# Kernel tuning notes

Measured on AMD Instinct MI355X. Metric: run time of the kernel, lower is better.

The kernel has to match this reference:

```python
import jax, jax.numpy as jnp
import numpy as np
from jax import lax

B, L = 8, 1024
C_IN, D_MODEL = 3, 512
N_MAMBA, N_TRANS, NHEAD = 2, 2, 8
D_STATE, D_CONV, EXPAND = 16, 4, 2
DI = EXPAND * D_MODEL            # 1024, mamba inner dim
DT_RANK = D_MODEL // 16          # 32
DH = D_MODEL // NHEAD            # 64, head dim
DFF = 4 * D_MODEL


def setup_inputs() -> dict:
    key = jax.random.key(0)
    ks = iter(jax.random.split(key, 64))
    def rn(shape, s=0.05):
        return jax.random.normal(next(ks), shape, jnp.float32) * s
    inp = {
        'x': jax.random.normal(next(ks), (B, C_IN, L), jnp.float32),
        'proj_w': rn((D_MODEL, C_IN)), 'proj_b': rn((D_MODEL,)),
        # stacked per-mamba-layer params (leading dim = N_MAMBA)
        'm_in_w': rn((N_MAMBA, 2 * DI, D_MODEL)),
        'm_conv_w': rn((N_MAMBA, DI, D_CONV)), 'm_conv_b': rn((N_MAMBA, DI)),
        'm_xproj_w': rn((N_MAMBA, DT_RANK + 2 * D_STATE, DI)),
        'm_dt_w': rn((N_MAMBA, DI, DT_RANK)), 'm_dt_b': rn((N_MAMBA, DI)),
        'm_Alog': jnp.tile(jnp.log(jnp.arange(1, D_STATE + 1, dtype=jnp.float32)), (N_MAMBA, DI, 1)),
        'm_D': jnp.ones((N_MAMBA, DI), jnp.float32),
        'm_out_w': rn((N_MAMBA, D_MODEL, DI)),
        'm_ln_w': jnp.ones((N_MAMBA, D_MODEL), jnp.float32), 'm_ln_b': jnp.zeros((N_MAMBA, D_MODEL), jnp.float32),
        # stacked per-transformer-layer params
        't_qkv_w': rn((N_TRANS, 3 * D_MODEL, D_MODEL)), 't_qkv_b': rn((N_TRANS, 3 * D_MODEL)),
        't_ow': rn((N_TRANS, D_MODEL, D_MODEL)), 't_ob': rn((N_TRANS, D_MODEL)),
        't_l1w': rn((N_TRANS, DFF, D_MODEL)), 't_l1b': rn((N_TRANS, DFF)),
        't_l2w': rn((N_TRANS, D_MODEL, DFF)), 't_l2b': rn((N_TRANS, D_MODEL)),
        't_ln1w': jnp.ones((N_TRANS, D_MODEL), jnp.float32), 't_ln1b': jnp.zeros((N_TRANS, D_MODEL), jnp.float32),
        't_ln2w': jnp.ones((N_TRANS, D_MODEL), jnp.float32), 't_ln2b': jnp.zeros((N_TRANS, D_MODEL), jnp.float32),
        'no_w': jnp.ones((D_MODEL,), jnp.float32), 'no_b': jnp.zeros((D_MODEL,), jnp.float32),
    }
    return inp


def _ln(x, w, b, eps=1e-5):
    m = x.mean(-1, keepdims=True)
    v = ((x - m) ** 2).mean(-1, keepdims=True)
    return (x - m) / jnp.sqrt(v + eps) * w + b


def _pos_encoding(length, d):
    pos = jnp.arange(length, dtype=jnp.float32)[:, None]
    div = jnp.exp(jnp.arange(0, d, 2, dtype=jnp.float32) * (-np.log(10000.0) / d))
    pe = jnp.zeros((length, d), jnp.float32)
    pe = pe.at[:, 0::2].set(jnp.sin(pos * div)).at[:, 1::2].set(jnp.cos(pos * div))
    return pe


def _mamba(h, in_w, conv_w, conv_b, xp_w, dt_w, dt_b, Alog, Dp, out_w):
    # h: [B,L,d_model]
    xz = h @ in_w.T                                   # [B,L,2*DI]
    xm, z = jnp.split(xz, 2, axis=-1)
    # causal depthwise conv1d over time
    k = conv_w.T[:, None, :]                          # [D_CONV,1,DI]
    xc = lax.conv_general_dilated(xm, k, (1,), [(D_CONV - 1, 0)],
                                  dimension_numbers=('NWC', 'WIO', 'NWC'),
                                  feature_group_count=DI) + conv_b
    xc = jax.nn.silu(xc)
    xdb = xc @ xp_w.T                                 # [B,L,DT_RANK+2*D_STATE]
    dt = jax.nn.softplus(xdb[..., :DT_RANK] @ dt_w.T + dt_b)   # [B,L,DI]
    Bm = xdb[..., DT_RANK:DT_RANK + D_STATE]          # [B,L,D_STATE]
    Cm = xdb[..., DT_RANK + D_STATE:]                 # [B,L,D_STATE]
    A = -jnp.exp(Alog)                                # [DI,D_STATE]

    def step(state, t):
        dt_t, B_t, C_t, x_t = t                       # [B,DI],[B,S],[B,S],[B,DI]
        dA = jnp.exp(dt_t[..., None] * A)             # [B,DI,S]
        state = state * dA + (dt_t * x_t)[..., None] * B_t[:, None, :]
        y = jnp.einsum('bds,bs->bd', state, C_t)
        return state, y

    init = jnp.zeros((h.shape[0], DI, D_STATE), h.dtype)
    seq = (dt.transpose(1, 0, 2), Bm.transpose(1, 0, 2), Cm.transpose(1, 0, 2), xc.transpose(1, 0, 2))
    _, ys = lax.scan(step, init, seq)                 # ys: [L,B,DI]
    y = ys.transpose(1, 0, 2) + Dp * xc
    y = y * jax.nn.silu(z)
    return y @ out_w.T                                # [B,L,d_model]


def _transformer_layer(h, qkv_w, qkv_b, ow, ob, l1w, l1b, l2w, l2b, ln1w, ln1b, ln2w, ln2b):
    Bt, Lt, d = h.shape
    qkv = h @ qkv_w.T + qkv_b
    q, k, v = jnp.split(qkv, 3, axis=-1)
    q = q.reshape(Bt, Lt, NHEAD, DH); k = k.reshape(Bt, Lt, NHEAD, DH); v = v.reshape(Bt, Lt, NHEAD, DH)
    sc = jnp.einsum('blhd,bmhd->bhlm', q, k) / np.sqrt(DH).astype(np.float32)
    a = jax.nn.softmax(sc, axis=-1)
    o = jnp.einsum('bhlm,bmhd->blhd', a, v).reshape(Bt, Lt, d)
    h = _ln(h + o @ ow.T + ob, ln1w, ln1b)
    ff = jax.nn.relu(h @ l1w.T + l1b) @ l2w.T + l2b
    return _ln(h + ff, ln2w, ln2b)


def reference(x, proj_w, proj_b, m_in_w, m_conv_w, m_conv_b, m_xproj_w, m_dt_w, m_dt_b,
              m_Alog, m_D, m_out_w, m_ln_w, m_ln_b, t_qkv_w, t_qkv_b, t_ow, t_ob,
              t_l1w, t_l1b, t_l2w, t_l2b, t_ln1w, t_ln1b, t_ln2w, t_ln2b, no_w, no_b):
    # proj_in: 1x1 conv == pointwise linear over channels; output [B,L,d]
    h = jnp.einsum('bcl,dc->bld', x, proj_w) + proj_b
    for i in range(N_MAMBA):
        h = _ln(h + _mamba(h, m_in_w[i], m_conv_w[i], m_conv_b[i], m_xproj_w[i],
                           m_dt_w[i], m_dt_b[i], m_Alog[i], m_D[i], m_out_w[i]),
                m_ln_w[i], m_ln_b[i])
    h = h + _pos_encoding(h.shape[1], D_MODEL)
    for i in range(N_TRANS):
        h = _transformer_layer(h, t_qkv_w[i], t_qkv_b[i], t_ow[i], t_ob[i],
                               t_l1w[i], t_l1b[i], t_l2w[i], t_l2b[i],
                               t_ln1w[i], t_ln1b[i], t_ln2w[i], t_ln2b[i])
    h = _ln(h, no_w, no_b)
    return h, h.mean(axis=1)
```

## Files before the change

kernel.cpp:

```cpp
#include <hip/hip_runtime.h>
#include <cstddef>

#define BATCH 8
#define LSEQ 1024
#define DMODEL 512
#define DINNER 1024
#define DSTATE 16
#define DTRANK 32
#define NHEAD 8
#define DHEAD 64
#define DFF 2048
#define MTOK 8192
#define NCHUNK 16
#define CLEN 64

typedef __attribute__((ext_vector_type(8))) short bfrag;
typedef __attribute__((ext_vector_type(4))) float f32x4;
typedef __attribute__((ext_vector_type(4))) unsigned short us4;
typedef unsigned short ushort_t;

__device__ __forceinline__ float silu_f(float x) { return x / (1.f + __expf(-x)); }

__device__ __forceinline__ unsigned short f2bf(float f) {
  unsigned u = __float_as_uint(f);
  return (unsigned short)((u + 0x7FFFu + ((u >> 16) & 1u)) >> 16);
}
__device__ __forceinline__ float bf2f(ushort_t u) {
  return __uint_as_float((unsigned)u << 16);
}

__device__ __forceinline__ void gll16(const ushort_t* g, ushort_t* l) {
  __builtin_amdgcn_global_load_lds(
      (const __attribute__((address_space(1))) unsigned int*)g,
      (__attribute__((address_space(3))) unsigned int*)l, 16, 0, 0);
}

__global__ __launch_bounds__(256) void cvt_bf16(const float* __restrict__ s,
                                                ushort_t* __restrict__ d, int n4) {
  int i = blockIdx.x * 256 + threadIdx.x;
  if (i >= n4) return;
  float4 v = ((const float4*)s)[i];
  us4 o = {f2bf(v.x), f2bf(v.y), f2bf(v.z), f2bf(v.w)};
  ((us4*)d)[i] = o;
}

__global__ __launch_bounds__(256) void proj_kernel(const float* __restrict__ x,
                                                   const float* __restrict__ pw,
                                                   const float* __restrict__ pb,
                                                   float* __restrict__ h,
                                                   ushort_t* __restrict__ hbf) {
  int idx = blockIdx.x * 256 + threadIdx.x;
  int d = idx & 511;
  int l = (idx >> 9) & 1023;
  int b = idx >> 19;
  const float* xb = x + (size_t)b * 3 * 1024 + l;
  float v = pb[d] + xb[0] * pw[d * 3] + xb[1024] * pw[d * 3 + 1] + xb[2048] * pw[d * 3 + 2];
  h[idx] = v;
  hbf[idx] = f2bf(v);
}

template <int ACT, int CBF, int SPLITK, int BN>
__global__ __launch_bounds__(256) void gemm_gll(const ushort_t* __restrict__ A,
                                                const ushort_t* __restrict__ W,
                                                const float* __restrict__ bias,
                                                void* __restrict__ Cp,
                                                int K, int lda, int ldc) {
  __shared__ ushort_t sA[2][4096];
  __shared__ ushort_t sB[2][BN * 32];
  constexpr int MREP = (BN == 128) ? 4 : 2;
  const int bm = blockIdx.y * 128, bn = blockIdx.x * BN;
  const int tid = threadIdx.x;
  const int wid = tid >> 6, lane = tid & 63;
  const int wrb = (BN == 128) ? (wid >> 1) * 64 : wid * 32;
  const int wcb = (BN == 128) ? (wid & 1) * 64 : 0;
  const int lr = lane & 15, ls = lane >> 4;
  const int sw = ls ^ ((lr >> 1) & 3);

  const int kseg = K / SPLITK;
  const int kbeg = (SPLITK > 1) ? blockIdx.z * kseg : 0;

  const int c0 = wid * 128 + lane;
  const int c1 = c0 + 64;
  const int r0 = c0 >> 2, s0 = (c0 & 3) ^ ((r0 >> 1) & 3);
  const int r1 = c1 >> 2, s1 = (c1 & 3) ^ ((r1 >> 1) & 3);
  const ushort_t* gA0 = A + (size_t)(bm + r0) * lda + kbeg + s0 * 8;
  const ushort_t* gA1 = A + (size_t)(bm + r1) * lda + kbeg + s1 * 8;
  const ushort_t* gB0;
  const ushort_t* gB1 = nullptr;
  if constexpr (BN == 128) {
    gB0 = W + (size_t)(bn + r0) * K + kbeg + s0 * 8;
    gB1 = W + (size_t)(bn + r1) * K + kbeg + s1 * 8;
  } else {
    const int cb = wid * 64 + lane;
    const int rb = cb >> 2, sb2 = (cb & 3) ^ ((rb >> 1) & 3);
    gB0 = W + (size_t)(bn + rb) * K + kbeg + sb2 * 8;
  }

  f32x4 acc[MREP][4];
#pragma unroll
  for (int i = 0; i < MREP; ++i)
#pragma unroll
    for (int j = 0; j < 4; ++j) acc[i][j] = (f32x4)(0.f);

#define STAGE(buf, step)                                             \
  do {                                                               \
    gll16(gA0 + (step) * 32, &sA[buf][wid * 1024]);                  \
    gll16(gA1 + (step) * 32, &sA[buf][wid * 1024 + 512]);            \
    if constexpr (BN == 128) {                                       \
      gll16(gB0 + (step) * 32, &sB[buf][wid * 1024]);                \
      gll16(gB1 + (step) * 32, &sB[buf][wid * 1024 + 512]);          \
    } else {                                                         \
      gll16(gB0 + (step) * 32, &sB[buf][wid * 512]);                 \
    }                                                                \
  } while (0)

  const int NT = kseg / 32;
  STAGE(0, 0);
  for (int t = 0; t < NT; ++t) {
    const int cur = t & 1;
    if (t + 1 < NT) {
      STAGE(cur ^ 1, t + 1);
      if constexpr (BN == 128)
        asm volatile("s_waitcnt vmcnt(4)" ::: "memory");
      else
        asm volatile("s_waitcnt vmcnt(3)" ::: "memory");
    } else {
      asm volatile("s_waitcnt vmcnt(0)" ::: "memory");
    }
    __builtin_amdgcn_sched_barrier(0);
    __builtin_amdgcn_s_barrier();
    __builtin_amdgcn_sched_barrier(0);

    bfrag af[MREP], bf[4];
#pragma unroll
    for (int mi = 0; mi < MREP; ++mi) {
      int row = wrb + mi * 16 + lr;
      af[mi] = *(const bfrag*)&sA[cur][(size_t)((row << 2) + sw) * 8];
    }
#pragma unroll
    for (int nj = 0; nj < 4; ++nj) {
      int col = wcb + nj * 16 + lr;
      bf[nj] = *(const bfrag*)&sB[cur][(size_t)((col << 2) + sw) * 8];
    }
#pragma unroll
    for (int mi = 0; mi < MREP; ++mi)
#pragma unroll
      for (int nj = 0; nj < 4; ++nj)
        acc[mi][nj] = __builtin_amdgcn_mfma_f32_16x16x32_bf16(af[mi], bf[nj], acc[mi][nj], 0, 0, 0);

    __builtin_amdgcn_s_barrier();
    __builtin_amdgcn_sched_barrier(0);
  }
#undef STAGE

  if (SPLITK > 1) {
    float* Cz = (float*)Cp + (size_t)blockIdx.z * 8192 * ldc;
#pragma unroll
    for (int nj = 0; nj < 4; ++nj) {
      int col = bn + wcb + nj * 16 + lr;
#pragma unroll
      for (int mi = 0; mi < MREP; ++mi) {
        int row0 = bm + wrb + mi * 16 + ls * 4;
#pragma unroll
        for (int r = 0; r < 4; ++r)
          Cz[(size_t)(row0 + r) * ldc + col] = acc[mi][nj][r];
      }
    }
  } else {
#pragma unroll
    for (int nj = 0; nj < 4; ++nj) {
      int col = bn + wcb + nj * 16 + lr;
      float bv = bias ? bias[col] : 0.f;
#pragma unroll
      for (int mi = 0; mi < MREP; ++mi) {
        int row0 = bm + wrb + mi * 16 + ls * 4;
#pragma unroll
        for (int r = 0; r < 4; ++r) {
          float v = acc[mi][nj][r] + bv;
          if (ACT == 1) v = fmaxf(v, 0.f);
          if (ACT == 2) v = (v > 20.f) ? v : log1pf(__expf(v));
          if (CBF)
            ((ushort_t*)Cp)[(size_t)(row0 + r) * ldc + col] = f2bf(v);
          else
            ((float*)Cp)[(size_t)(row0 + r) * ldc + col] = v;
        }
      }
    }
  }
}

__global__ __launch_bounds__(256) void splitk_reduce(const float* __restrict__ p,
                                                     const float* __restrict__ bias,
                                                     float* __restrict__ out) {
  int i = blockIdx.x * 256 + threadIdx.x;
  float4 a = ((const float4*)p)[i];
  float4 b = ((const float4*)p)[i + 1048576];
  float4 o = {a.x + b.x, a.y + b.y, a.z + b.z, a.w + b.w};
  if (bias) {
    float4 bb = ((const float4*)bias)[i & 127];
    o.x += bb.x; o.y += bb.y; o.z += bb.z; o.w += bb.w;
  }
  ((float4*)out)[i] = o;
}

__global__ __launch_bounds__(256) void reduce8_xdb(const float* __restrict__ p,
                                                   float* __restrict__ xdb,
                                                   ushort_t* __restrict__ xdb_bf) {
  int i = blockIdx.x * 256 + threadIdx.x;
  float4 a = ((const float4*)p)[i];
#pragma unroll
  for (int z = 1; z < 8; ++z) {
    float4 b = ((const float4*)p)[i + z * 131072];
    a.x += b.x; a.y += b.y; a.z += b.z; a.w += b.w;
  }
  ((float4*)xdb)[i] = a;
  us4 o = {f2bf(a.x), f2bf(a.y), f2bf(a.z), f2bf(a.w)};
  ((us4*)xdb_bf)[i] = o;
}

__global__ __launch_bounds__(256) void conv_silu_kernel(const float* __restrict__ xz,
                                                        const float* __restrict__ cw,
                                                        const float* __restrict__ cb,
                                                        ushort_t* __restrict__ xc) {
  int idx = blockIdx.x * 256 + threadIdx.x;
  int d = idx & 1023;
  int t = (idx >> 10) & 1023;
  int b = idx >> 20;
  float acc = cb[d];
#pragma unroll
  for (int w = 0; w < 4; ++w) {
    int tt = t - 3 + w;
    if (tt >= 0) acc += xz[(((size_t)(b * 1024 + tt)) << 11) + d] * cw[d * 4 + w];
  }
  xc[idx] = f2bf(silu_f(acc));
}

__global__ __launch_bounds__(256) void scan_pass1(const float* __restrict__ dt,
                                                  const float* __restrict__ xdb,
                                                  const ushort_t* __restrict__ xc,
                                                  const float* __restrict__ Alog,
                                                  float* __restrict__ scrP,
                                                  float* __restrict__ scrL) {
  int idx = blockIdx.x * 256 + threadIdx.x;
  int sh = idx & 3;
  int d = (idx >> 2) & 1023;
  int c = (idx >> 12) & 15;
  int b = idx >> 16;
  float A[4], st[4], P[4];
#pragma unroll
  for (int s = 0; s < 4; ++s) {
    A[s] = -__expf(Alog[d * 16 + sh * 4 + s]);
    st[s] = 0.f;
    P[s] = 1.f;
  }
  int t0 = c * CLEN;
  size_t base = (((size_t)(b * 1024 + t0)) << 10) + d;
  const float* xb = xdb + (size_t)(b * 1024 + t0) * 64 + 32 + sh * 4;
  float dtv = dt[base], xv = bf2f(xc[base]);
  for (int t = 0; t < CLEN; ++t) {
    float dtn = 0.f, xvn = 0.f;
    if (t + 1 < CLEN) { dtn = dt[base + 1024]; xvn = bf2f(xc[base + 1024]); }
    float4 Bv = *(const float4*)xb;
    float dx = dtv * xv;
    float e0 = __expf(dtv * A[0]), e1 = __expf(dtv * A[1]);
    float e2 = __expf(dtv * A[2]), e3 = __expf(dtv * A[3]);
    st[0] = st[0] * e0 + dx * Bv.x; P[0] *= e0;
    st[1] = st[1] * e1 + dx * Bv.y; P[1] *= e1;
    st[2] = st[2] * e2 + dx * Bv.z; P[2] *= e2;
    st[3] = st[3] * e3 + dx * Bv.w; P[3] *= e3;
    base += 1024; xb += 64;
    dtv = dtn; xv = xvn;
  }
  size_t pbase = (((size_t)((b * 16 + c) * 16 + sh * 4)) << 10) + d;
#pragma unroll
  for (int s = 0; s < 4; ++s) {
    scrP[pbase + ((size_t)s << 10)] = P[s];
    scrL[pbase + ((size_t)s << 10)] = st[s];
  }
}

__global__ __launch_bounds__(256) void scan_pass2(const float* __restrict__ scrP,
                                                  float* __restrict__ scrL) {
  int idx = blockIdx.x * 256 + threadIdx.x;
  int d = idx & 1023;
  int s = (idx >> 10) & 15;
  int b = idx >> 14;
  float cur = 0.f;
  for (int c = 0; c < 16; ++c) {
    size_t o = (((size_t)(((b * 16 + c) * 16) + s)) << 10) + d;
    float P = scrP[o];
    float loc = scrL[o];
    scrL[o] = cur;
    cur = cur * P + loc;
  }
}

__global__ __launch_bounds__(256) void scan_pass3(const float* __restrict__ dt,
                                                  const float* __restrict__ xdb,
                                                  const ushort_t* __restrict__ xc,
                                                  const float* __restrict__ xz,
                                                  ushort_t* __restrict__ ybf,
                                                  const float* __restrict__ Alog,
                                                  const float* __restrict__ Dp,
                                                  const float* __restrict__ scrL) {
  int idx = blockIdx.x * 256 + threadIdx.x;
  int sh = idx & 3;
  int d = (idx >> 2) & 1023;
  int c = (idx >> 12) & 15;
  int b = idx >> 16;
  float A[4], st[4];
  size_t pbase = (((size_t)((b * 16 + c) * 16 + sh * 4)) << 10) + d;
#pragma unroll
  for (int s = 0; s < 4; ++s) {
    A[s] = -__expf(Alog[d * 16 + sh * 4 + s]);
    st[s] = scrL[pbase + ((size_t)s << 10)];
  }
  float Dv = Dp[d];
  int t0 = c * CLEN;
  size_t base = (((size_t)(b * 1024 + t0)) << 10) + d;
  size_t zoff = ((((size_t)(b * 1024 + t0)) << 11)) + 1024 + d;
  const float* xb = xdb + (size_t)(b * 1024 + t0) * 64 + 32 + sh * 4;
  float dtv = dt[base], xv = bf2f(xc[base]), zv = xz[zoff];
  for (int t = 0; t < CLEN; ++t) {
    float dtn = 0.f, xvn = 0.f, zvn = 0.f;
    if (t + 1 < CLEN) {
      dtn = dt[base + 1024]; xvn = bf2f(xc[base + 1024]); zvn = xz[zoff + 2048];
    }
    float4 Bv = *(const float4*)xb;
    float4 Cv = *(const float4*)(xb + 16);
    float dx = dtv * xv;
    float e0 = __expf(dtv * A[0]), e1 = __expf(dtv * A[1]);
    float e2 = __expf(dtv * A[2]), e3 = __expf(dtv * A[3]);
    st[0] = st[0] * e0 + dx * Bv.x;
    st[1] = st[1] * e1 + dx * Bv.y;
    st[2] = st[2] * e2 + dx * Bv.z;
    st[3] = st[3] * e3 + dx * Bv.w;
    float acc = st[0] * Cv.x + st[1] * Cv.y + st[2] * Cv.z + st[3] * Cv.w;
    acc += __shfl_xor(acc, 1);
    acc += __shfl_xor(acc, 2);
    if (sh == 0)
      ybf[base] = f2bf((acc + Dv * xv) * silu_f(zv));
    base += 1024; zoff += 2048; xb += 64;
    dtv = dtn; xv = xvn; zv = zvn;
  }
}

__global__ __launch_bounds__(128) void resid_ln_kernel(const float* __restrict__ x,
                                                       const float* __restrict__ add,
                                                       const float* __restrict__ w,
                                                       const float* __restrict__ bias,
                                                       float* __restrict__ out,
                                                       ushort_t* __restrict__ out_bf) {
  int row = blockIdx.x, tid = threadIdx.x;
  float4 v = ((const float4*)(x + (size_t)row * 512))[tid];
  if (add) {
    float4 a = ((const float4*)(add + (size_t)row * 512))[tid];
    v.x += a.x; v.y += a.y; v.z += a.z; v.w += a.w;
  }
  float s = v.x + v.y + v.z + v.w;
  float ss = v.x * v.x + v.y * v.y + v.z * v.z + v.w * v.w;
#pragma unroll
  for (int o = 32; o; o >>= 1) {
    s += __shfl_xor(s, o);
    ss += __shfl_xor(ss, o);
  }
  __shared__ float red[4];
  int wid = tid >> 6;
  if ((tid & 63) == 0) { red[wid] = s; red[2 + wid] = ss; }
  __syncthreads();
  s = red[0] + red[1];
  ss = red[2] + red[3];
  float mean = s * (1.f / 512.f);
  float var = ss * (1.f / 512.f) - mean * mean;
  float inv = rsqrtf(var + 1e-5f);
  float4 wv = ((const float4*)w)[tid];
  float4 bv = ((const float4*)bias)[tid];
  float4 ov;
  ov.x = (v.x - mean) * inv * wv.x + bv.x;
  ov.y = (v.y - mean) * inv * wv.y + bv.y;
  ov.z = (v.z - mean) * inv * wv.z + bv.z;
  ov.w = (v.w - mean) * inv * wv.w + bv.w;
  ((float4*)(out + (size_t)row * 512))[tid] = ov;
  if (out_bf) {
    us4 ob = {f2bf(ov.x), f2bf(ov.y), f2bf(ov.z), f2bf(ov.w)};
    ((us4*)(out_bf + (size_t)row * 512))[tid] = ob;
  }
}

__global__ __launch_bounds__(256) void posenc_kernel(float* __restrict__ h,
                                                     ushort_t* __restrict__ hbf) {
  int idx = blockIdx.x * 256 + threadIdx.x;
  int d = idx & 511;
  int l = (idx >> 9) & 1023;
  float freq = __expf(-(float)(d & ~1) * (9.210340371976184f / 512.f));
  float ang = (float)l * freq;
  float v = h[idx] + ((d & 1) ? cosf(ang) : sinf(ang));
  h[idx] = v;
  hbf[idx] = f2bf(v);
}

__global__ __launch_bounds__(256) void attn_mfma(const ushort_t* __restrict__ qkv,
                                                 ushort_t* __restrict__ ao) {
  __shared__ unsigned short Qs[4096];
  __shared__ unsigned short Ks[4096];
  __shared__ unsigned short Vt[4096];
  __shared__ unsigned short Ps[4096];
  const int tid = threadIdx.x;
  const int blk = blockIdx.x;
  const int qt = blk & 15, hh = (blk >> 4) & 7, b = blk >> 7;
  const int l0 = qt * 64;
  const size_t bb = (size_t)b * 1024 * 1536;

  const int srow = tid >> 2;
  const int sdb = (tid & 3) << 4;
  const int sc0 = sdb >> 3;

  {
    const ushort_t* qp = qkv + bb + (size_t)(l0 + srow) * 1536 + hh * 64 + sdb;
    *(bfrag*)&Qs[srow * 64 + ((sc0 ^ (srow & 7)) << 3)] = *(const bfrag*)qp;
    *(bfrag*)&Qs[srow * 64 + (((sc0 + 1) ^ (srow & 7)) << 3)] = *(const bfrag*)(qp + 8);
  }

  const int wid = tid >> 6, lane = tid & 63;
  const int l15 = lane & 15, rg = lane >> 4;
  const int l7 = l15 & 7;
  float m[4], lsum[4];
  f32x4 oacc[4];
#pragma unroll
  for (int r = 0; r < 4; ++r) { m[r] = -1e30f; lsum[r] = 0.f; }
#pragma unroll
  for (int nt = 0; nt < 4; ++nt) oacc[nt] = (f32x4)(0.f);

  for (int jt = 0; jt < 16; ++jt) {
    {
      const ushort_t* kp = qkv + bb + (size_t)(jt * 64 + srow) * 1536 + hh * 64 + 512 + sdb;
      *(bfrag*)&Ks[srow * 64 + ((sc0 ^ (srow & 7)) << 3)] = *(const bfrag*)kp;
      *(bfrag*)&Ks[srow * 64 + (((sc0 + 1) ^ (srow & 7)) << 3)] = *(const bfrag*)(kp + 8);
      const ushort_t* vp = kp + 512;
      unsigned short vv[16];
      *(bfrag*)&vv[0] = *(const bfrag*)vp;
      *(bfrag*)&vv[8] = *(const bfrag*)(vp + 8);
#pragma unroll
      for (int j = 0; j < 16; ++j) {
        int dd = sdb + j;
        Vt[dd * 64 + (((srow >> 3) ^ (dd & 7)) << 3) + (srow & 7)] = vv[j];
      }
    }
    __syncthreads();

    bfrag aq[2];
#pragma unroll
    for (int ks = 0; ks < 2; ++ks)
      aq[ks] = *(const bfrag*)&Qs[(wid * 16 + l15) * 64 + (((ks * 4 + rg) ^ l7) << 3)];
    f32x4 sc[4];
#pragma unroll
    for (int nt = 0; nt < 4; ++nt) {
      f32x4 s = (f32x4)(0.f);
#pragma unroll
      for (int ks = 0; ks < 2; ++ks) {
        bfrag bk = *(const bfrag*)&Ks[(nt * 16 + l15) * 64 + (((ks * 4 + rg) ^ l7) << 3)];
        s = __builtin_amdgcn_mfma_f32_16x16x32_bf16(aq[ks], bk, s, 0, 0, 0);
      }
      sc[nt] = s * 0.125f;
    }

#pragma unroll
    for (int r = 0; r < 4; ++r) {
      float mc = fmaxf(fmaxf(sc[0][r], sc[1][r]), fmaxf(sc[2][r], sc[3][r]));
#pragma unroll
      for (int o = 8; o; o >>= 1) mc = fmaxf(mc, __shfl_xor(mc, o));
      float mn = fmaxf(m[r], mc);
      float al = __expf(m[r] - mn);
      m[r] = mn;
      int prow = rg * 4 + r;
      float ps = 0.f;
#pragma unroll
      for (int nt = 0; nt < 4; ++nt) {
        float p = __expf(sc[nt][r] - mn);
        ps += p;
        int col = nt * 16 + l15;
        Ps[wid * 1024 + prow * 64 + ((((col >> 3) ^ (prow & 7))) << 3) + (col & 7)] = f2bf(p);
      }
#pragma unroll
      for (int o = 8; o; o >>= 1) ps += __shfl_xor(ps, o);
      lsum[r] = lsum[r] * al + ps;
#pragma unroll
      for (int nt = 0; nt < 4; ++nt) oacc[nt][r] *= al;
    }

    bfrag ap[2];
#pragma unroll
    for (int ks = 0; ks < 2; ++ks)
      ap[ks] = *(const bfrag*)&Ps[wid * 1024 + l15 * 64 + (((ks * 4 + rg) ^ l7) << 3)];
#pragma unroll
    for (int nt = 0; nt < 4; ++nt) {
#pragma unroll
      for (int ks = 0; ks < 2; ++ks) {
        bfrag bv = *(const bfrag*)&Vt[(nt * 16 + l15) * 64 + (((ks * 4 + rg) ^ l7) << 3)];
        oacc[nt] = __builtin_amdgcn_mfma_f32_16x16x32_bf16(ap[ks], bv, oacc[nt], 0, 0, 0);
      }
    }
    __syncthreads();
  }

#pragma unroll
  for (int r = 0; r < 4; ++r) {
    float inv = 1.f / lsum[r];
    int row = l0 + wid * 16 + rg * 4 + r;
    ushort_t* op = ao + ((size_t)(b * 1024 + row)) * 512 + hh * 64;
#pragma unroll
    for (int nt = 0; nt < 4; ++nt) op[nt * 16 + l15] = f2bf(oacc[nt][r] * inv);
  }
}

__global__ __launch_bounds__(512) void mean_part(const float* __restrict__ h,
                                                 float* __restrict__ part) {
  int blk = blockIdx.x;
  int b = blk >> 4, lc = blk & 15, d = threadIdx.x;
  float s = 0.f;
  int l0 = lc * 64;
  for (int l = l0; l < l0 + 64; ++l) s += h[(((size_t)(b * 1024 + l)) << 9) + d];
  part[((size_t)blk << 9) + d] = s;
}
__global__ __launch_bounds__(256) void mean_final(const float* __restrict__ part,
                                                  float* __restrict__ out2) {
  int i = blockIdx.x * 256 + threadIdx.x;
  int b = i >> 9, d = i & 511;
  float s = 0.f;
#pragma unroll
  for (int c = 0; c < 16; ++c) s += part[(((size_t)(b * 16 + c)) << 9) + d];
  out2[i] = s * (1.f / 1024.f);
}

extern "C" void kernel_launch(void* const* d_in, const int* in_sizes, int n_in,
                              void* d_out, int out_size, void* d_ws, size_t ws_size,
                              hipStream_t stream) {
  const float* x        = (const float*)d_in[0];
  const float* proj_w   = (const float*)d_in[1];
  const float* proj_b   = (const float*)d_in[2];
  const float* m_in_w   = (const float*)d_in[3];
  const float* m_conv_w = (const float*)d_in[4];
  const float* m_conv_b = (const float*)d_in[5];
  const float* m_xproj_w= (const float*)d_in[6];
  const float* m_dt_w   = (const float*)d_in[7];
  const float* m_dt_b   = (const float*)d_in[8];
  const float* m_Alog   = (const float*)d_in[9];
  const float* m_D      = (const float*)d_in[10];
  const float* m_out_w  = (const float*)d_in[11];
  const float* m_ln_w   = (const float*)d_in[12];
  const float* m_ln_b   = (const float*)d_in[13];
  const float* t_qkv_w  = (const float*)d_in[14];
  const float* t_qkv_b  = (const float*)d_in[15];
  const float* t_ow     = (const float*)d_in[16];
  const float* t_ob     = (const float*)d_in[17];
  const float* t_l1w    = (const float*)d_in[18];
  const float* t_l1b    = (const float*)d_in[19];
  const float* t_l2w    = (const float*)d_in[20];
  const float* t_l2b    = (const float*)d_in[21];
  const float* t_ln1w   = (const float*)d_in[22];
  const float* t_ln1b   = (const float*)d_in[23];
  const float* t_ln2w   = (const float*)d_in[24];
  const float* t_ln2b   = (const float*)d_in[25];
  const float* no_w     = (const float*)d_in[26];
  const float* no_b     = (const float*)d_in[27];

  float* ws   = (float*)d_ws;
  float* h    = ws;
  ushort_t* h_bf = (ushort_t*)(ws + 4194304);
  float* bufA = ws + 6291456;
  float* bufB = bufA + 16777216;
  float* bufC = bufB + 8388608;
  float* bufE = bufC + 8388608;
  float* bufF = bufE + 4194304;
  ushort_t* y_bf = (ushort_t*)(bufF + 524288);
  ushort_t* wbf  = (ushort_t*)(bufF + 524288 + 4194304);
  float* scrP = bufE;
  float* scrL = bufE + 2097152;

  ushort_t* wIN  = wbf;
  ushort_t* wOUT = wbf + 2097152;
  ushort_t* wQKV = wbf + 3145728;
  ushort_t* wOW  = wbf + 4718592;
  ushort_t* wL1  = wbf + 5242880;
  ushort_t* wL2  = wbf + 7340032;
  ushort_t* wXP  = wbf + 9437184;
  ushort_t* wDT  = wbf + 9568256;
  ushort_t* xdb_bf = wbf + 9633792;

  cvt_bf16<<<2048, 256, 0, stream>>>(m_in_w,  wIN,  524288);
  cvt_bf16<<<1024, 256, 0, stream>>>(m_out_w, wOUT, 262144);
  cvt_bf16<<<1536, 256, 0, stream>>>(t_qkv_w, wQKV, 393216);
  cvt_bf16<<< 512, 256, 0, stream>>>(t_ow,    wOW,  131072);
  cvt_bf16<<<2048, 256, 0, stream>>>(t_l1w,   wL1,  524288);
  cvt_bf16<<<2048, 256, 0, stream>>>(t_l2w,   wL2,  524288);
  cvt_bf16<<< 128, 256, 0, stream>>>(m_xproj_w, wXP, 32768);
  cvt_bf16<<<  64, 256, 0, stream>>>(m_dt_w,  wDT,  16384);

  proj_kernel<<<16384, 256, 0, stream>>>(x, proj_w, proj_b, h, h_bf);

  for (int i = 0; i < 2; ++i) {
    gemm_gll<0, 0, 1, 128><<<dim3(16, 64), 256, 0, stream>>>(
        h_bf, wIN + (size_t)i * 1048576, nullptr, bufA, DMODEL, DMODEL, 2 * DINNER);
    conv_silu_kernel<<<32768, 256, 0, stream>>>(bufA, m_conv_w + i * DINNER * 4,
                                                m_conv_b + i * DINNER, (ushort_t*)bufB);
    gemm_gll<0, 0, 8, 64><<<dim3(1, 64, 8), 256, 0, stream>>>(
        (const ushort_t*)bufB, wXP + (size_t)i * 65536, nullptr, bufC,
        DINNER, DINNER, 64);
    reduce8_xdb<<<512, 256, 0, stream>>>(bufC, bufF, xdb_bf);
    gemm_gll<2, 0, 1, 128><<<dim3(8, 64), 256, 0, stream>>>(
        xdb_bf, wDT + (size_t)i * 32768, m_dt_b + i * DINNER, bufC,
        DTRANK, 64, DINNER);
    scan_pass1<<<2048, 256, 0, stream>>>(bufC, bufF, (const ushort_t*)bufB,
                                         m_Alog + (size_t)i * DINNER * DSTATE, scrP, scrL);
    scan_pass2<<<512, 256, 0, stream>>>(scrP, scrL);
    scan_pass3<<<2048, 256, 0, stream>>>(bufC, bufF, (const ushort_t*)bufB, bufA, y_bf,
                                         m_Alog + (size_t)i * DINNER * DSTATE,
                                         m_D + i * DINNER, scrL);
    gemm_gll<0, 0, 2, 128><<<dim3(4, 64, 2), 256, 0, stream>>>(
        y_bf, wOUT + (size_t)i * 524288, nullptr, bufC, DINNER, DINNER, DMODEL);
    splitk_reduce<<<4096, 256, 0, stream>>>(bufC, nullptr, bufE);
    resid_ln_kernel<<<8192, 128, 0, stream>>>(h, bufE, m_ln_w + i * DMODEL,
                                              m_ln_b + i * DMODEL, h, h_bf);
  }

  posenc_kernel<<<16384, 256, 0, stream>>>(h, h_bf);

  for (int i = 0; i < 2; ++i) {
    gemm_gll<0, 1, 1, 128><<<dim3(12, 64), 256, 0, stream>>>(
        h_bf, wQKV + (size_t)i * 786432, t_qkv_b + i * 3 * DMODEL, bufA,
        DMODEL, DMODEL, 3 * DMODEL);
    attn_mfma<<<1024, 256, 0, stream>>>((const ushort_t*)bufA, (ushort_t*)bufB);
    gemm_gll<0, 0, 2, 128><<<dim3(4, 64, 2), 256, 0, stream>>>(
        (const ushort_t*)bufB, wOW + (size_t)i * 262144, nullptr, bufC,
        DMODEL, DMODEL, DMODEL);
    splitk_reduce<<<4096, 256, 0, stream>>>(bufC, t_ob + i * DMODEL, bufE);
    resid_ln_kernel<<<8192, 128, 0, stream>>>(h, bufE, t_ln1w + i * DMODEL,
                                              t_ln1b + i * DMODEL, h, h_bf);
    gemm_gll<1, 1, 1, 128><<<dim3(16, 64), 256, 0, stream>>>(
        h_bf, wL1 + (size_t)i * 1048576, t_l1b + i * DFF, bufA,
        DMODEL, DMODEL, DFF);
    gemm_gll<0, 0, 2, 128><<<dim3(4, 64, 2), 256, 0, stream>>>(
        (const ushort_t*)bufA, wL2 + (size_t)i * 1048576, nullptr, bufC,
        DFF, DFF, DMODEL);
    splitk_reduce<<<4096, 256, 0, stream>>>(bufC, t_l2b + i * DMODEL, bufE);
    resid_ln_kernel<<<8192, 128, 0, stream>>>(h, bufE, t_ln2w + i * DMODEL,
                                              t_ln2b + i * DMODEL, h, h_bf);
  }

  float* out_h = (float*)d_out;
  resid_ln_kernel<<<8192, 128, 0, stream>>>(h, nullptr, no_w, no_b, out_h, nullptr);
  mean_part<<<128, 512, 0, stream>>>(out_h, bufF);
  mean_final<<<16, 256, 0, stream>>>(bufF, out_h + 4194304);
}
```

Measured before the change: 987.4 us.

## Fuse split-K reduce into residual LayerNorm, store in_proj as bf16, widen attention tiles

The separate split-K reduction kernel is removed. Its two partial sums and the bias are now added inside a new residual-LayerNorm kernel, which saves one full-size write and read of the activation per linear layer. The Mamba in_proj GEMM now writes bf16 instead of fp32, so the conv and scan kernels read half the bytes, at the cost of rounding the gate and input values. The attention kernel now handles 128 query rows per block with each wave covering two 16-row sub-tiles, so every K/V tile loaded into shared memory is reused twice. This uses more registers and launches half as many blocks.

Measured after the change: 963.8 us. 1.02x faster.

```diff
diff --git a/kernel.cpp b/kernel.cpp
--- a/kernel.cpp
+++ b/kernel.cpp
@@ -189,20 +189,6 @@
   }
 }
 
-__global__ __launch_bounds__(256) void splitk_reduce(const float* __restrict__ p,
-                                                     const float* __restrict__ bias,
-                                                     float* __restrict__ out) {
-  int i = blockIdx.x * 256 + threadIdx.x;
-  float4 a = ((const float4*)p)[i];
-  float4 b = ((const float4*)p)[i + 1048576];
-  float4 o = {a.x + b.x, a.y + b.y, a.z + b.z, a.w + b.w};
-  if (bias) {
-    float4 bb = ((const float4*)bias)[i & 127];
-    o.x += bb.x; o.y += bb.y; o.z += bb.z; o.w += bb.w;
-  }
-  ((float4*)out)[i] = o;
-}
-
 __global__ __launch_bounds__(256) void reduce8_xdb(const float* __restrict__ p,
                                                    float* __restrict__ xdb,
                                                    ushort_t* __restrict__ xdb_bf) {
@@ -218,7 +204,7 @@
   ((us4*)xdb_bf)[i] = o;
 }
 
-__global__ __launch_bounds__(256) void conv_silu_kernel(const float* __restrict__ xz,
+__global__ __launch_bounds__(256) void conv_silu_kernel(const ushort_t* __restrict__ xz,
                                                         const float* __restrict__ cw,
                                                         const float* __restrict__ cb,
                                                         ushort_t* __restrict__ xc) {
@@ -230,7 +216,7 @@
 #pragma unroll
   for (int w = 0; w < 4; ++w) {
     int tt = t - 3 + w;
-    if (tt >= 0) acc += xz[(((size_t)(b * 1024 + tt)) << 11) + d] * cw[d * 4 + w];
+    if (tt >= 0) acc += bf2f(xz[(((size_t)(b * 1024 + tt)) << 11) + d]) * cw[d * 4 + w];
   }
   xc[idx] = f2bf(silu_f(acc));
 }
@@ -298,7 +284,7 @@
 __global__ __launch_bounds__(256) void scan_pass3(const float* __restrict__ dt,
                                                   const float* __restrict__ xdb,
                                                   const ushort_t* __restrict__ xc,
-                                                  const float* __restrict__ xz,
+                                                  const ushort_t* __restrict__ xz,
                                                   ushort_t* __restrict__ ybf,
                                                   const float* __restrict__ Alog,
                                                   const float* __restrict__ Dp,
@@ -320,11 +306,11 @@
   size_t base = (((size_t)(b * 1024 + t0)) << 10) + d;
   size_t zoff = ((((size_t)(b * 1024 + t0)) << 11)) + 1024 + d;
   const float* xb = xdb + (size_t)(b * 1024 + t0) * 64 + 32 + sh * 4;
-  float dtv = dt[base], xv = bf2f(xc[base]), zv = xz[zoff];
+  float dtv = dt[base], xv = bf2f(xc[base]), zv = bf2f(xz[zoff]);
   for (int t = 0; t < CLEN; ++t) {
     float dtn = 0.f, xvn = 0.f, zvn = 0.f;
     if (t + 1 < CLEN) {
-      dtn = dt[base + 1024]; xvn = bf2f(xc[base + 1024]); zvn = xz[zoff + 2048];
+      dtn = dt[base + 1024]; xvn = bf2f(xc[base + 1024]); zvn = bf2f(xz[zoff + 2048]);
     }
     float4 Bv = *(const float4*)xb;
     float4 Cv = *(const float4*)(xb + 16);
@@ -387,6 +373,50 @@
   }
 }
 
+__global__ __launch_bounds__(128) void resid_ln_sk(const float* __restrict__ x,
+                                                   const float* __restrict__ p,
+                                                   const float* __restrict__ pbias,
+                                                   const float* __restrict__ w,
+                                                   const float* __restrict__ bias,
+                                                   float* __restrict__ out,
+                                                   ushort_t* __restrict__ out_bf) {
+  int row = blockIdx.x, tid = threadIdx.x;
+  float4 v = ((const float4*)(x + (size_t)row * 512))[tid];
+  float4 a = ((const float4*)(p + (size_t)row * 512))[tid];
+  float4 c = ((const float4*)(p + 4194304 + (size_t)row * 512))[tid];
+  v.x += a.x + c.x; v.y += a.y + c.y; v.z += a.z + c.z; v.w += a.w + c.w;
+  if (pbias) {
+    float4 pb = ((const float4*)pbias)[tid];
+    v.x += pb.x; v.y += pb.y; v.z += pb.z; v.w += pb.w;
+  }
+  float s = v.x + v.y + v.z + v.w;
+  float ss = v.x * v.x + v.y * v.y + v.z * v.z + v.w * v.w;
+#pragma unroll
+  for (int o = 32; o; o >>= 1) {
+    s += __shfl_xor(s, o);
+    ss += __shfl_xor(ss, o);
+  }
+  __shared__ float red[4];
+  int wid = tid >> 6;
+  if ((tid & 63) == 0) { red[wid] = s; red[2 + wid] = ss; }
+  __syncthreads();
+  s = red[0] + red[1];
+  ss = red[2] + red[3];
+  float mean = s * (1.f / 512.f);
+  float var = ss * (1.f / 512.f) - mean * mean;
+  float inv = rsqrtf(var + 1e-5f);
+  float4 wv = ((const float4*)w)[tid];
+  float4 bv = ((const float4*)bias)[tid];
+  float4 ov;
+  ov.x = (v.x - mean) * inv * wv.x + bv.x;
+  ov.y = (v.y - mean) * inv * wv.y + bv.y;
+  ov.z = (v.z - mean) * inv * wv.z + bv.z;
+  ov.w = (v.w - mean) * inv * wv.w + bv.w;
+  ((float4*)(out + (size_t)row * 512))[tid] = ov;
+  us4 ob = {f2bf(ov.x), f2bf(ov.y), f2bf(ov.z), f2bf(ov.w)};
+  ((us4*)(out_bf + (size_t)row * 512))[tid] = ob;
+}
+
 __global__ __launch_bounds__(256) void posenc_kernel(float* __restrict__ h,
                                                      ushort_t* __restrict__ hbf) {
   int idx = blockIdx.x * 256 + threadIdx.x;
@@ -401,14 +431,14 @@
 
 __global__ __launch_bounds__(256) void attn_mfma(const ushort_t* __restrict__ qkv,
                                                  ushort_t* __restrict__ ao) {
-  __shared__ unsigned short Qs[4096];
+  __shared__ unsigned short Qs[8192];
   __shared__ unsigned short Ks[4096];
   __shared__ unsigned short Vt[4096];
   __shared__ unsigned short Ps[4096];
   const int tid = threadIdx.x;
   const int blk = blockIdx.x;
-  const int qt = blk & 15, hh = (blk >> 4) & 7, b = blk >> 7;
-  const int l0 = qt * 64;
+  const int qt = blk & 7, hh = (blk >> 3) & 7, b = blk >> 6;
+  const int l0 = qt * 128;
   const size_t bb = (size_t)b * 1024 * 1536;
 
   const int srow = tid >> 2;
@@ -419,17 +449,35 @@
     const ushort_t* qp = qkv + bb + (size_t)(l0 + srow) * 1536 + hh * 64 + sdb;
     *(bfrag*)&Qs[srow * 64 + ((sc0 ^ (srow & 7)) << 3)] = *(const bfrag*)qp;
     *(bfrag*)&Qs[srow * 64 + (((sc0 + 1) ^ (srow & 7)) << 3)] = *(const bfrag*)(qp + 8);
-  }
+    const ushort_t* qp2 = qp + (size_t)64 * 1536;
+    *(bfrag*)&Qs[(srow + 64) * 64 + ((sc0 ^ (srow & 7)) << 3)] = *(const bfrag*)qp2;
+    *(bfrag*)&Qs[(srow + 64) * 64 + (((sc0 + 1) ^ (srow & 7)) << 3)] = *(const bfrag*)(qp2 + 8);
+  }
+  __syncthreads();
 
   const int wid = tid >> 6, lane = tid & 63;
   const int l15 = lane & 15, rg = lane >> 4;
   const int l7 = l15 & 7;
-  float m[4], lsum[4];
-  f32x4 oacc[4];
-#pragma unroll
-  for (int r = 0; r < 4; ++r) { m[r] = -1e30f; lsum[r] = 0.f; }
-#pragma unroll
-  for (int nt = 0; nt < 4; ++nt) oacc[nt] = (f32x4)(0.f);
+
+  bfrag aq[2][2];
+#pragma unroll
+  for (int s = 0; s < 2; ++s)
+#pragma unroll
+    for (int ks = 0; ks < 2; ++ks) {
+      int qr = wid * 32 + s * 16 + l15;
+      aq[s][ks] = *(const bfrag*)&Qs[qr * 64 + (((ks * 4 + rg) ^ l7) << 3)];
+    }
+
+  float m[2][4], lsum[2][4];
+  f32x4 oacc[2][4];
+#pragma unroll
+  for (int s = 0; s < 2; ++s)
+#pragma unroll
+    for (int r = 0; r < 4; ++r) { m[s][r] = -1e30f; lsum[s][r] = 0.f; }
+#pragma unroll
+  for (int s = 0; s < 2; ++s)
+#pragma unroll
+    for (int nt = 0; nt < 4; ++nt) oacc[s][nt] = (f32x4)(0.f);
 
   for (int jt = 0; jt < 16; ++jt) {
     {
@@ -448,69 +496,70 @@
     }
     __syncthreads();
 
-    bfrag aq[2];
-#pragma unroll
-    for (int ks = 0; ks < 2; ++ks)
-      aq[ks] = *(const bfrag*)&Qs[(wid * 16 + l15) * 64 + (((ks * 4 + rg) ^ l7) << 3)];
-    f32x4 sc[4];
-#pragma unroll
-    for (int nt = 0; nt < 4; ++nt) {
-      f32x4 s = (f32x4)(0.f);
-#pragma unroll
-      for (int ks = 0; ks < 2; ++ks) {
-        bfrag bk = *(const bfrag*)&Ks[(nt * 16 + l15) * 64 + (((ks * 4 + rg) ^ l7) << 3)];
-        s = __builtin_amdgcn_mfma_f32_16x16x32_bf16(aq[ks], bk, s, 0, 0, 0);
+#pragma unroll
+    for (int s = 0; s < 2; ++s) {
+      f32x4 sc[4];
+#pragma unroll
+      for (int nt = 0; nt < 4; ++nt) {
+        f32x4 sv = (f32x4)(0.f);
+#pragma unroll
+        for (int ks = 0; ks < 2; ++ks) {
+          bfrag bk = *(const bfrag*)&Ks[(nt * 16 + l15) * 64 + (((ks * 4 + rg) ^ l7) << 3)];
+          sv = __builtin_amdgcn_mfma_f32_16x16x32_bf16(aq[s][ks], bk, sv, 0, 0, 0);
+        }
+        sc[nt] = sv * 0.125f;
       }
-      sc[nt] = s * 0.125f;
-    }
-
+
+#pragma unroll
+      for (int r = 0; r < 4; ++r) {
+        float mc = fmaxf(fmaxf(sc[0][r], sc[1][r]), fmaxf(sc[2][r], sc[3][r]));
+#pragma unroll
+        for (int o = 8; o; o >>= 1) mc = fmaxf(mc, __shfl_xor(mc, o));
+        float mn = fmaxf(m[s][r], mc);
+        float al = __expf(m[s][r] - mn);
+        m[s][r] = mn;
+        int prow = rg * 4 + r;
+        float ps = 0.f;
+#pragma unroll
+        for (int nt = 0; nt < 4; ++nt) {
+          float p = __expf(sc[nt][r] - mn);
+          ps += p;
+          int col = nt * 16 + l15;
+          Ps[wid * 1024 + prow * 64 + ((((col >> 3) ^ (prow & 7))) << 3) + (col & 7)] = f2bf(p);
+        }
+#pragma unroll
+        for (int o = 8; o; o >>= 1) ps += __shfl_xor(ps, o);
+        lsum[s][r] = lsum[s][r] * al + ps;
+#pragma unroll
+        for (int nt = 0; nt < 4; ++nt) oacc[s][nt][r] *= al;
+      }
+
+      bfrag ap[2];
+#pragma unroll
+      for (int ks = 0; ks < 2; ++ks)
+        ap[ks] = *(const bfrag*)&Ps[wid * 1024 + l15 * 64 + (((ks * 4 + rg) ^ l7) << 3)];
+#pragma unroll
+      for (int nt = 0; nt < 4; ++nt) {
+#pragma unroll
+        for (int ks = 0; ks < 2; ++ks) {
+          bfrag bv = *(const bfrag*)&Vt[(nt * 16 + l15) * 64 + (((ks * 4 + rg) ^ l7) << 3)];
+          oacc[s][nt] = __builtin_amdgcn_mfma_f32_16x16x32_bf16(ap[ks], bv, oacc[s][nt], 0, 0, 0);
+        }
+      }
+    }
+    __syncthreads();
+  }
+
+#pragma unroll
+  for (int s = 0; s < 2; ++s)
 #pragma unroll
     for (int r = 0; r < 4; ++r) {
-      float mc = fmaxf(fmaxf(sc[0][r], sc[1][r]), fmaxf(sc[2][r], sc[3][r]));
-#pragma unroll
-      for (int o = 8; o; o >>= 1) mc = fmaxf(mc, __shfl_xor(mc, o));
-      float mn = fmaxf(m[r], mc);
-      float al = __expf(m[r] - mn);
-      m[r] = mn;
-      int prow = rg * 4 + r;
-      float ps = 0.f;
-#pragma unroll
-      for (int nt = 0; nt < 4; ++nt) {
-        float p = __expf(sc[nt][r] - mn);
-        ps += p;
-        int col = nt * 16 + l15;
-        Ps[wid * 1024 + prow * 64 + ((((col >> 3) ^ (prow & 7))) << 3) + (col & 7)] = f2bf(p);
-      }
-#pragma unroll
-      for (int o = 8; o; o >>= 1) ps += __shfl_xor(ps, o);
-      lsum[r] = lsum[r] * al + ps;
-#pragma unroll
-      for (int nt = 0; nt < 4; ++nt) oacc[nt][r] *= al;
-    }
-
-    bfrag ap[2];
-#pragma unroll
-    for (int ks = 0; ks < 2; ++ks)
-      ap[ks] = *(const bfrag*)&Ps[wid * 1024 + l15 * 64 + (((ks * 4 + rg) ^ l7) << 3)];
-#pragma unroll
-    for (int nt = 0; nt < 4; ++nt) {
-#pragma unroll
-      for (int ks = 0; ks < 2; ++ks) {
-        bfrag bv = *(const bfrag*)&Vt[(nt * 16 + l15) * 64 + (((ks * 4 + rg) ^ l7) << 3)];
-        oacc[nt] = __builtin_amdgcn_mfma_f32_16x16x32_bf16(ap[ks], bv, oacc[nt], 0, 0, 0);
-      }
-    }
-    __syncthreads();
-  }
-
-#pragma unroll
-  for (int r = 0; r < 4; ++r) {
-    float inv = 1.f / lsum[r];
-    int row = l0 + wid * 16 + rg * 4 + r;
-    ushort_t* op = ao + ((size_t)(b * 1024 + row)) * 512 + hh * 64;
-#pragma unroll
-    for (int nt = 0; nt < 4; ++nt) op[nt * 16 + l15] = f2bf(oacc[nt][r] * inv);
-  }
+      float inv = 1.f / lsum[s][r];
+      int row = l0 + wid * 32 + s * 16 + rg * 4 + r;
+      ushort_t* op = ao + ((size_t)(b * 1024 + row)) * 512 + hh * 64;
+#pragma unroll
+      for (int nt = 0; nt < 4; ++nt) op[nt * 16 + l15] = f2bf(oacc[s][nt][r] * inv);
+    }
 }
 
 __global__ __launch_bounds__(512) void mean_part(const float* __restrict__ h,
@@ -599,9 +648,10 @@
   proj_kernel<<<16384, 256, 0, stream>>>(x, proj_w, proj_b, h, h_bf);
 
   for (int i = 0; i < 2; ++i) {
-    gemm_gll<0, 0, 1, 128><<<dim3(16, 64), 256, 0, stream>>>(
+    gemm_gll<0, 1, 1, 128><<<dim3(16, 64), 256, 0, stream>>>(
         h_bf, wIN + (size_t)i * 1048576, nullptr, bufA, DMODEL, DMODEL, 2 * DINNER);
-    conv_silu_kernel<<<32768, 256, 0, stream>>>(bufA, m_conv_w + i * DINNER * 4,
+    conv_silu_kernel<<<32768, 256, 0, stream>>>((const ushort_t*)bufA,
+                                                m_conv_w + i * DINNER * 4,
                                                 m_conv_b + i * DINNER, (ushort_t*)bufB);
     gemm_gll<0, 0, 8, 64><<<dim3(1, 64, 8), 256, 0, stream>>>(
         (const ushort_t*)bufB, wXP + (size_t)i * 65536, nullptr, bufC,
@@ -613,14 +663,14 @@
     scan_pass1<<<2048, 256, 0, stream>>>(bufC, bufF, (const ushort_t*)bufB,
                                          m_Alog + (size_t)i * DINNER * DSTATE, scrP, scrL);
     scan_pass2<<<512, 256, 0, stream>>>(scrP, scrL);
-    scan_pass3<<<2048, 256, 0, stream>>>(bufC, bufF, (const ushort_t*)bufB, bufA, y_bf,
+    scan_pass3<<<2048, 256, 0, stream>>>(bufC, bufF, (const ushort_t*)bufB,
+                                         (const ushort_t*)bufA, y_bf,
                                          m_Alog + (size_t)i * DINNER * DSTATE,
                                          m_D + i * DINNER, scrL);
     gemm_gll<0, 0, 2, 128><<<dim3(4, 64, 2), 256, 0, stream>>>(
         y_bf, wOUT + (size_t)i * 524288, nullptr, bufC, DINNER, DINNER, DMODEL);
-    splitk_reduce<<<4096, 256, 0, stream>>>(bufC, nullptr, bufE);
-    resid_ln_kernel<<<8192, 128, 0, stream>>>(h, bufE, m_ln_w + i * DMODEL,
-                                              m_ln_b + i * DMODEL, h, h_bf);
+    resid_ln_sk<<<8192, 128, 0, stream>>>(h, bufC, nullptr, m_ln_w + i * DMODEL,
+                                          m_ln_b + i * DMODEL, h, h_bf);
   }
 
   posenc_kernel<<<16384, 256, 0, stream>>>(h, h_bf);
@@ -629,22 +679,20 @@
     gemm_gll<0, 1, 1, 128><<<dim3(12, 64), 256, 0, stream>>>(
         h_bf, wQKV + (size_t)i * 786432, t_qkv_b + i * 3 * DMODEL, bufA,
         DMODEL, DMODEL, 3 * DMODEL);
-    attn_mfma<<<1024, 256, 0, stream>>>((const ushort_t*)bufA, (ushort_t*)bufB);
+    attn_mfma<<<512, 256, 0, stream>>>((const ushort_t*)bufA, (ushort_t*)bufB);
     gemm_gll<0, 0, 2, 128><<<dim3(4, 64, 2), 256, 0, stream>>>(
         (const ushort_t*)bufB, wOW + (size_t)i * 262144, nullptr, bufC,
         DMODEL, DMODEL, DMODEL);
-    splitk_reduce<<<4096, 256, 0, stream>>>(bufC, t_ob + i * DMODEL, bufE);
-    resid_ln_kernel<<<8192, 128, 0, stream>>>(h, bufE, t_ln1w + i * DMODEL,
-                                              t_ln1b + i * DMODEL, h, h_bf);
+    resid_ln_sk<<<8192, 128, 0, stream>>>(h, bufC, t_ob + i * DMODEL,
+                                          t_ln1w + i * DMODEL, t_ln1b + i * DMODEL, h, h_bf);
     gemm_gll<1, 1, 1, 128><<<dim3(16, 64), 256, 0, stream>>>(
         h_bf, wL1 + (size_t)i * 1048576, t_l1b + i * DFF, bufA,
         DMODEL, DMODEL, DFF);
     gemm_gll<0, 0, 2, 128><<<dim3(4, 64, 2), 256, 0, stream>>>(
         (const ushort_t*)bufA, wL2 + (size_t)i * 1048576, nullptr, bufC,
         DFF, DFF, DMODEL);
-    splitk_reduce<<<4096, 256, 0, stream>>>(bufC, t_l2b + i * DMODEL, bufE);
-    resid_ln_kernel<<<8192, 128, 0, stream>>>(h, bufE, t_ln2w + i * DMODEL,
-                                              t_ln2b + i * DMODEL, h, h_bf);
+    resid_ln_sk<<<8192, 128, 0, stream>>>(h, bufC, t_l2b + i * DMODEL,
+                                          t_ln2w + i * DMODEL, t_ln2b + i * DMODEL, h, h_bf);
   }
 
   float* out_h = (float*)d_out;
```
